# Performance work log

Hardware: AMD Instinct MI355X
Metric: run time of the kernel (lower is better)

Reference implementation:

```python
import jax, jax.numpy as jnp
import numpy as np

EPS = 1e-5

def _bn(x, g, b):
    # BatchNorm3d in training mode over (batch, spatial) dims; x: [B, C, N]
    mean = jnp.mean(x, axis=(0, 2), keepdims=True)
    var = jnp.var(x, axis=(0, 2), keepdims=True)
    return g[None, :, None] * (x - mean) * jax.lax.rsqrt(var + EPS) + b[None, :, None]


def setup_inputs() -> dict:
    key = jax.random.key(0)
    ks = jax.random.split(key, 6)
    B, C, N, K, H = 2, 128, 32768, 9, 512
    x = jax.random.normal(ks[0], (B, C, N, 1), dtype=jnp.float32)
    edge_index = jax.random.randint(ks[1], (2, B, N, K), 0, N, dtype=jnp.int32)
    s = 0.05
    return {
        "x": x,
        "edge_index": edge_index,
        "w_mr": jax.random.normal(ks[2], (C, 2 * C), dtype=jnp.float32) * s,
        "b_mr": jnp.zeros((C,), jnp.float32),
        "g_mr": jnp.ones((C,), jnp.float32),
        "be_mr": jnp.zeros((C,), jnp.float32),
        "w1": jax.random.normal(ks[3], (H, C), dtype=jnp.float32) * s,
        "b1": jnp.zeros((H,), jnp.float32),
        "g1": jnp.ones((H,), jnp.float32),
        "be1": jnp.zeros((H,), jnp.float32),
        "w2": jax.random.normal(ks[4], (C, H), dtype=jnp.float32) * s,
        "b2": jnp.zeros((C,), jnp.float32),
        "g2": jnp.ones((C,), jnp.float32),
        "be2": jnp.zeros((C,), jnp.float32),
    }


def reference(x, edge_index, w_mr, b_mr, g_mr, be_mr, w1, b1, g1, be1, w2, b2, g2, be2):
    # x: [B, C, N, 1], edge_index: [2, B, N, K]
    B, C, N, _ = x.shape
    x2 = x[..., 0]  # [B, C, N]

    # batched_index_select: gather node features along N for each (B, N, K) index
    gather = jax.vmap(lambda xb, ib: xb[:, ib])  # ([C,N],[N,K]) -> [C,N,K]
    x_i = gather(x2, edge_index[1])  # [B, C, N, K] center features
    x_j = gather(x2, edge_index[0])  # [B, C, N, K] neighbor features
    rel = jnp.max(x_j - x_i, axis=-1)  # max-relative reduction -> [B, C, N]

    # torch.cat([x.unsqueeze(2), rel.unsqueeze(2)], 2).reshape(B, 2C, N): interleaved channels
    feat = jnp.stack([x2, rel], axis=2).reshape(B, 2 * C, N)

    # BasicConv([2C, C]): Conv3d 1x1 -> BN -> ReLU
    y = jnp.einsum('oc,bcn->bon', w_mr, feat) + b_mr[None, :, None]
    y = jax.nn.relu(_bn(y, g_mr, be_mr))

    # FFN: conv1x1 C->H, BN, ReLU, conv1x1 H->C, BN, residual
    h = jnp.einsum('hc,bcn->bhn', w1, y) + b1[None, :, None]
    h = jax.nn.relu(_bn(h, g1, be1))
    out = jnp.einsum('ch,bhn->bcn', w2, h) + b2[None, :, None]
    out = _bn(out, g2, be2) + y
    return out  # [B, C, N]
```

## Files before the change

kernel.cpp:

```cpp
#include <hip/hip_runtime.h>
#include <hip/hip_bf16.h>
#include <cstddef>
#include <cstdint>

#define BB 2
#define CC 128
#define NN 32768
#define KNBR 9
#define HH 512
#define PP (BB * NN)
#define TWO_C 256
#define EPSBN 1e-5f

typedef __attribute__((ext_vector_type(4))) float f32x4;
typedef __attribute__((ext_vector_type(8))) short s16x8;

__device__ __forceinline__ float bf2f(unsigned int u) {
    return __uint_as_float(u << 16);
}
__device__ __forceinline__ unsigned short f2bf(float f) {
    unsigned int u = __float_as_uint(f);
    u += 0x7fffu + ((u >> 16) & 1u);
    return (unsigned short)(u >> 16);
}


__global__ __launch_bounds__(256) void transpose_kernel(
    const float* __restrict__ x, unsigned short* __restrict__ xT) {
    __shared__ float t[32][129];
    const int b = blockIdx.y;
    const int n0 = blockIdx.x * 32;
    const int tid = threadIdx.x;
    {
        const int tn = tid % 32;
        const int cq = tid / 32;
        for (int c = cq; c < CC; c += 8)
            t[tn][c] = x[((size_t)b * CC + c) * NN + n0 + tn];
    }
    __syncthreads();
    {
        const int ct = tid % 128;
        const int nq = tid / 128;
        for (int nl = nq; nl < 32; nl += 2)
            xT[((size_t)b * NN + n0 + nl) * CC + ct] = f2bf(t[nl][ct]);
    }
}

__global__ __launch_bounds__(256) void gather_kernel(
    const unsigned short* __restrict__ xT, const int* __restrict__ ei,
    unsigned short* __restrict__ feat) {
    __shared__ unsigned short lds[16 * 264];
    const int p0 = blockIdx.x * 16;
    const int b = p0 >> 15;
    const int n0 = p0 & (NN - 1);
    const int tid = threadIdx.x;
    const int wv = tid >> 6, lane = tid & 63;
    const unsigned short* xb = xT + (size_t)b * NN * CC;

#pragma unroll
    for (int q = 0; q < 4; q++) {
        const int pl = wv * 4 + q;
        const int n = n0 + pl;
        const int* e0 = ei + ((size_t)b * NN + n) * KNBR;
        const int* e1 = ei + ((size_t)(BB + b) * NN + n) * KNBR;
        const unsigned int xv = *(const unsigned int*)(xb + (size_t)n * CC + lane * 2);
        float m0 = -INFINITY, m1 = -INFINITY;
#pragma unroll
        for (int k = 0; k < KNBR; k++) {
            const int j0 = e0[k], j1 = e1[k];
            const unsigned int va = *(const unsigned int*)(xb + (size_t)j0 * CC + lane * 2);
            const unsigned int vb = *(const unsigned int*)(xb + (size_t)j1 * CC + lane * 2);
            m0 = fmaxf(m0, bf2f(va & 0xffffu) - bf2f(vb & 0xffffu));
            m1 = fmaxf(m1, bf2f(va >> 16) - bf2f(vb >> 16));
        }
        ushort4 o;
        o.x = (unsigned short)(xv & 0xffffu);
        o.y = f2bf(m0);
        o.z = (unsigned short)(xv >> 16);
        o.w = f2bf(m1);
        *(ushort4*)(lds + pl * 264 + lane * 4) = o;
    }
    __syncthreads();
#pragma unroll
    for (int pass = 0; pass < 2; pass++) {
        const int s = pass * 256 + tid;
        const int kt = s >> 6, ln = s & 63;
        const int pl = ln & 15, kq = ln >> 4;
        const s16x8 v = *(const s16x8*)(lds + pl * 264 + kt * 32 + kq * 8);
        *(s16x8*)(feat + ((size_t)((p0 >> 4) * 8 + kt) * 64 + ln) * 8) = v;
    }
}

__global__ __launch_bounds__(256) void wconv_kernel(
    const float* __restrict__ w_mr, const float* __restrict__ w1,
    const float* __restrict__ w2, unsigned short* __restrict__ o_mr,
    unsigned short* __restrict__ o1, unsigned short* __restrict__ o2) {
    const int t = blockIdx.x * 256 + threadIdx.x;
    const float* src; unsigned short* dst; int K; int slot;
    if (t < 8192) { src = w1; dst = o1; K = 128; slot = t; }
    else if (t < 16384) { src = w2; dst = o2; K = 512; slot = t - 8192; }
    else if (t < 20480) { src = w_mr; dst = o_mr; K = 256; slot = t - 16384; }
    else return;
    const int lane = slot & 63;
    const int kt = (slot >> 6) % (K / 32);
    const int ot = (slot >> 6) / (K / 32);
    const int oc = ot * 16 + (lane & 15);
    const int k0 = kt * 32 + (lane >> 4) * 8;
    s16x8 v;
#pragma unroll
    for (int j = 0; j < 8; j++) v[j] = (short)f2bf(src[(size_t)oc * K + k0 + j]);
    *(s16x8*)(dst + (size_t)slot * 8) = v;
}

template <int KTOT, int OC, bool ACT>
__global__ __launch_bounds__(256) void fgemm_kernel(
    const unsigned short* __restrict__ A,
    const unsigned short* __restrict__ W,
    const float* __restrict__ bias,
    const float* __restrict__ act,
    unsigned short* __restrict__ Cout,
    float* __restrict__ stats) {
    constexpr int KT = KTOT / 32;
    constexpr int OCT = OC / 32;
    __shared__ unsigned short ctile[4][2][64][8];
    __shared__ float bsA[256], bsB[256];

    const int tid = threadIdx.x;
    const int pb = blockIdx.x * 128;
    const int ob = blockIdx.y * 128;
    const int w = tid >> 6, wr = w >> 1, wc = w & 1;
    const int lane = tid & 63;
    const int lm = lane & 15, lg = lane >> 4;

    const unsigned short* Abase =
        A + ((size_t)((pb >> 4) + wr * 4) * KT * 64 + lane) * 8;
    const unsigned short* Wbase =
        W + ((size_t)((ob >> 4) + wc * 4) * KT * 64 + lane) * 8;

    f32x4 acc[4][4] = {};

    for (int kt = 0; kt < KT; kt++) {
        s16x8 aF[4], bF[4];
#pragma unroll
        for (int n = 0; n < 4; n++)
            bF[n] = *(const s16x8*)(Wbase + ((size_t)n * KT + kt) * 512);
        f32x4 sa0, sa1, sb0, sb1;
        if (ACT) {
            const int ke = kt * 32 + lg * 8;
            sa0 = *(const f32x4*)(act + ke);
            sa1 = *(const f32x4*)(act + ke + 4);
            sb0 = *(const f32x4*)(act + KTOT + ke);
            sb1 = *(const f32x4*)(act + KTOT + ke + 4);
        }
#pragma unroll
        for (int m = 0; m < 4; m++) {
            s16x8 v = *(const s16x8*)(Abase + ((size_t)m * KT + kt) * 512);
            if (ACT) {
                union { s16x8 s; __hip_bfloat162 h[4]; } u;
                u.s = v;
#pragma unroll
                for (int q = 0; q < 4; q++) {
                    const float2 f = __bfloat1622float2(u.h[q]);
                    const float slo = (q < 2) ? sa0[2 * q] : sa1[2 * q - 4];
                    const float shi = (q < 2) ? sa0[2 * q + 1] : sa1[2 * q - 3];
                    const float tlo = (q < 2) ? sb0[2 * q] : sb1[2 * q - 4];
                    const float thi = (q < 2) ? sb0[2 * q + 1] : sb1[2 * q - 3];
                    const float rlo = fmaxf(fmaf(slo, f.x, tlo), 0.f);
                    const float rhi = fmaxf(fmaf(shi, f.y, thi), 0.f);
                    u.h[q] = __float22bfloat162_rn(make_float2(rlo, rhi));
                }
                v = u.s;
            }
            aF[m] = v;
        }
#pragma unroll
        for (int m = 0; m < 4; m++)
#pragma unroll
            for (int n = 0; n < 4; n++)
                acc[m][n] = __builtin_amdgcn_mfma_f32_16x16x32_bf16(
                    aF[m], bF[n], acc[m][n], 0, 0, 0);
    }

    float sA[4] = {0.f, 0.f, 0.f, 0.f};
    float sB[4] = {0.f, 0.f, 0.f, 0.f};
    float bo[4];
#pragma unroll
    for (int n = 0; n < 4; n++) bo[n] = bias[ob + wc * 64 + n * 16 + lm];
    const int octile0 = (ob >> 5) + wc * 2;
    const int elem = lm & 7;
#pragma unroll
    for (int m = 0; m < 4; m++) {
#pragma unroll
        for (int n = 0; n < 4; n++) {
            const int tile = n >> 1;
            const int lbase = ((n & 1) * 2 + (lm >> 3)) * 16 + lg * 4;
#pragma unroll
            for (int j = 0; j < 4; j++) {
                const float h = acc[m][n][j] + bo[n];
                sA[n] += h;
                sB[n] = fmaf(h, h, sB[n]);
                ctile[w][tile][lbase + j][elem] = f2bf(h);
            }
        }
        const int ptile = (pb >> 4) + wr * 4 + m;
#pragma unroll
        for (int tile = 0; tile < 2; tile++) {
            const s16x8 v = *(const s16x8*)&ctile[w][tile][lane][0];
            *(s16x8*)(Cout + ((size_t)(ptile * OCT + octile0 + tile) * 64 + lane) * 8) = v;
        }
    }
#pragma unroll
    for (int n = 0; n < 4; n++) {
        float a = sA[n], q = sB[n];
        a += __shfl_xor(a, 16); a += __shfl_xor(a, 32);
        q += __shfl_xor(q, 16); q += __shfl_xor(q, 32);
        if (lg == 0) {
            bsA[wr * 128 + wc * 64 + n * 16 + lm] = a;
            bsB[wr * 128 + wc * 64 + n * 16 + lm] = q;
        }
    }
    __syncthreads();
    if (tid < 128) {
        atomicAdd(&stats[ob + tid], bsA[tid] + bsA[128 + tid]);
        atomicAdd(&stats[OC + ob + tid], bsB[tid] + bsB[128 + tid]);
    }
}

__global__ void finalize_kernel(const float* __restrict__ stats,
                                const float* __restrict__ g,
                                const float* __restrict__ be,
                                float* __restrict__ act, int CH, float invP) {
    const int c = blockIdx.x * blockDim.x + threadIdx.x;
    if (c < CH) {
        const float mean = stats[c] * invP;
        const float var = stats[CH + c] * invP - mean * mean;
        const float a = g[c] * rsqrtf(var + EPSBN);
        act[c] = a;
        act[CH + c] = be[c] - mean * a;
    }
}

__global__ __launch_bounds__(256) void final_kernel(
    const unsigned short* __restrict__ yF, const unsigned short* __restrict__ oF,
    const float* __restrict__ act1, const float* __restrict__ act3,
    float* __restrict__ out) {
    __shared__ float t[32][132];
    const int p0 = blockIdx.x * 32;
    const int b = p0 >> 15;
    const int n0 = p0 & (NN - 1);
    const int tid = threadIdx.x;
#pragma unroll
    for (int s = tid; s < 512; s += 256) {
        const int pt = s >> 8;
        const int kt = (s >> 6) & 3;
        const int lane = s & 63;
        const int nl = pt * 16 + (lane & 15);
        const int c0 = kt * 32 + (lane >> 4) * 8;
        const size_t off = ((size_t)(((p0 >> 4) + pt) * 4 + kt) * 64 + lane) * 8;
        const s16x8 yv = *(const s16x8*)(yF + off);
        const s16x8 ov = *(const s16x8*)(oF + off);
        const f32x4 a1lo = *(const f32x4*)(act1 + c0);
        const f32x4 a1hi = *(const f32x4*)(act1 + c0 + 4);
        const f32x4 b1lo = *(const f32x4*)(act1 + CC + c0);
        const f32x4 b1hi = *(const f32x4*)(act1 + CC + c0 + 4);
        const f32x4 a3lo = *(const f32x4*)(act3 + c0);
        const f32x4 a3hi = *(const f32x4*)(act3 + c0 + 4);
        const f32x4 b3lo = *(const f32x4*)(act3 + CC + c0);
        const f32x4 b3hi = *(const f32x4*)(act3 + CC + c0 + 4);
#pragma unroll
        for (int j = 0; j < 8; j++) {
            const float yf = bf2f((unsigned short)yv[j]);
            const float of = bf2f((unsigned short)ov[j]);
            const float a1 = (j < 4) ? a1lo[j] : a1hi[j - 4];
            const float b1 = (j < 4) ? b1lo[j] : b1hi[j - 4];
            const float a3 = (j < 4) ? a3lo[j] : a3hi[j - 4];
            const float b3 = (j < 4) ? b3lo[j] : b3hi[j - 4];
            t[nl][c0 + j] = fmaf(a3, of, b3) + fmaxf(fmaf(a1, yf, b1), 0.f);
        }
    }
    __syncthreads();
    const int tn = tid & 31;
    const int cq = tid >> 5;
    for (int c = cq; c < CC; c += 8)
        out[((size_t)b * CC + c) * NN + n0 + tn] = t[tn][c];
}

extern "C" void kernel_launch(void* const* d_in, const int* in_sizes, int n_in,
                              void* d_out, int out_size, void* d_ws, size_t ws_size,
                              hipStream_t stream) {
    const float* x     = (const float*)d_in[0];
    const int*   ei    = (const int*)d_in[1];
    const float* w_mr  = (const float*)d_in[2];
    const float* b_mr  = (const float*)d_in[3];
    const float* g_mr  = (const float*)d_in[4];
    const float* be_mr = (const float*)d_in[5];
    const float* w1    = (const float*)d_in[6];
    const float* b1    = (const float*)d_in[7];
    const float* g1    = (const float*)d_in[8];
    const float* be1   = (const float*)d_in[9];
    const float* w2    = (const float*)d_in[10];
    const float* b2    = (const float*)d_in[11];
    const float* g2    = (const float*)d_in[12];
    const float* be2   = (const float*)d_in[13];
    float* out = (float*)d_out;

    char* ws = (char*)d_ws;
    unsigned short* xT    = (unsigned short*)(ws + 0);
    unsigned short* featF = (unsigned short*)(ws + 16777216);
    unsigned short* yF    = (unsigned short*)(ws + 50331648);
    unsigned short* hF    = (unsigned short*)(ws + 67108864);
    unsigned short* oF    = (unsigned short*)(ws + 134217728);
    unsigned short* wmrF  = (unsigned short*)(ws + 150994944);
    unsigned short* w1F   = (unsigned short*)(ws + 151060480);
    unsigned short* w2F   = (unsigned short*)(ws + 151191552);
    float* stats1 = (float*)(ws + 151322624);
    float* stats2 = (float*)(ws + 151323648);
    float* stats3 = (float*)(ws + 151327744);
    float* act1   = (float*)(ws + 151328768);
    float* act2   = (float*)(ws + 151329792);
    float* act3   = (float*)(ws + 151333888);

    const float invP = 1.0f / (float)PP;

    hipMemsetAsync(stats1, 0, 6144, stream);

    transpose_kernel<<<dim3(NN / 32, BB), 256, 0, stream>>>(x, xT);
    gather_kernel<<<PP / 16, 256, 0, stream>>>(xT, ei, featF);
    wconv_kernel<<<80, 256, 0, stream>>>(w_mr, w1, w2, wmrF, w1F, w2F);

    fgemm_kernel<TWO_C, CC, false><<<dim3(PP / 128, 1), 256, 0, stream>>>(
        featF, wmrF, b_mr, act1, yF, stats1);
    finalize_kernel<<<1, CC, 0, stream>>>(stats1, g_mr, be_mr, act1, CC, invP);

    fgemm_kernel<CC, HH, true><<<dim3(PP / 128, HH / 128), 256, 0, stream>>>(
        yF, w1F, b1, act1, hF, stats2);
    finalize_kernel<<<1, HH, 0, stream>>>(stats2, g1, be1, act2, HH, invP);

    fgemm_kernel<HH, CC, true><<<dim3(PP / 128, 1), 256, 0, stream>>>(
        hF, w2F, b2, act2, oF, stats3);
    finalize_kernel<<<1, CC, 0, stream>>>(stats3, g2, be2, act3, CC, invP);

    final_kernel<<<PP / 32, 256, 0, stream>>>(yF, oF, act1, act3, out);
}
```

Measured before the change: 176.7 us.

## Stage weights in LDS, retile GEMM warps, replace atomic BN stats with partial sums

Rewrites the fused GEMM so that each block stages its weight slice in shared memory and each wave owns two 16-row point tiles across the full output-channel block, with multiple M iterations per block. It also replaces the global atomicAdd BN statistics and memset with per-block partial sums reduced by a separate reduce kernel. The third GEMM restages weights per K-quarter with extra barriers. The aim is to cut redundant global weight loads and atomic contention, at the cost of more LDS usage, more synchronisation, and extra partial-sum memory traffic.

Result: slower. 256.4 us (+45.1%).

```diff
diff --git a/kernel.cpp b/kernel.cpp
--- a/kernel.cpp
+++ b/kernel.cpp
@@ -22,6 +22,23 @@
     unsigned int u = __float_as_uint(f);
     u += 0x7fffu + ((u >> 16) & 1u);
     return (unsigned short)(u >> 16);
+}
+
+__device__ __forceinline__ s16x8 bnrelu(s16x8 v, f32x4 sa0, f32x4 sa1,
+                                        f32x4 sb0, f32x4 sb1) {
+    union { s16x8 s; __hip_bfloat162 h[4]; } u;
+    u.s = v;
+#pragma unroll
+    for (int q = 0; q < 4; q++) {
+        const float2 f = __bfloat1622float2(u.h[q]);
+        const float slo = (q < 2) ? sa0[2 * q] : sa1[2 * q - 4];
+        const float shi = (q < 2) ? sa0[2 * q + 1] : sa1[2 * q - 3];
+        const float tlo = (q < 2) ? sb0[2 * q] : sb1[2 * q - 4];
+        const float thi = (q < 2) ? sb0[2 * q + 1] : sb1[2 * q - 3];
+        u.h[q] = __float22bfloat162_rn(make_float2(
+            fmaxf(fmaf(slo, f.x, tlo), 0.f), fmaxf(fmaf(shi, f.y, thi), 0.f)));
+    }
+    return u.s;
 }
 
 
@@ -112,131 +129,160 @@
     *(s16x8*)(dst + (size_t)slot * 8) = v;
 }
 
-template <int KTOT, int OC, bool ACT>
-__global__ __launch_bounds__(256) void fgemm_kernel(
+template <int KTOT, int OCB, int OC, bool ACT, bool RESTAGE, int MITERS>
+__global__ __launch_bounds__(256, 2) void wgemm_kernel(
     const unsigned short* __restrict__ A,
     const unsigned short* __restrict__ W,
     const float* __restrict__ bias,
     const float* __restrict__ act,
     unsigned short* __restrict__ Cout,
-    float* __restrict__ stats) {
+    float* __restrict__ part) {
     constexpr int KT = KTOT / 32;
-    constexpr int OCT = OC / 32;
-    __shared__ unsigned short ctile[4][2][64][8];
-    __shared__ float bsA[256], bsB[256];
+    constexpr int KQ = KT / 4;
+    constexpr int NT = OCB / 16;
+    constexpr int NT2 = NT / 2;
+    constexpr int WTILES = RESTAGE ? NT * 4 : NT * KT;
+    constexpr int OCT32 = OC / 32;
+    __shared__ __align__(16) unsigned short WL[WTILES * 512];
+    __shared__ __align__(16) unsigned short ctile[4][NT2][64][8];
+    __shared__ float bs[4][2][OCB];
 
     const int tid = threadIdx.x;
-    const int pb = blockIdx.x * 128;
-    const int ob = blockIdx.y * 128;
-    const int w = tid >> 6, wr = w >> 1, wc = w & 1;
+    const int w = tid >> 6;
     const int lane = tid & 63;
     const int lm = lane & 15, lg = lane >> 4;
-
-    const unsigned short* Abase =
-        A + ((size_t)((pb >> 4) + wr * 4) * KT * 64 + lane) * 8;
-    const unsigned short* Wbase =
-        W + ((size_t)((ob >> 4) + wc * 4) * KT * 64 + lane) * 8;
-
-    f32x4 acc[4][4] = {};
-
-    for (int kt = 0; kt < KT; kt++) {
-        s16x8 aF[4], bF[4];
-#pragma unroll
-        for (int n = 0; n < 4; n++)
-            bF[n] = *(const s16x8*)(Wbase + ((size_t)n * KT + kt) * 512);
-        f32x4 sa0, sa1, sb0, sb1;
-        if (ACT) {
-            const int ke = kt * 32 + lg * 8;
-            sa0 = *(const f32x4*)(act + ke);
-            sa1 = *(const f32x4*)(act + ke + 4);
-            sb0 = *(const f32x4*)(act + KTOT + ke);
-            sb1 = *(const f32x4*)(act + KTOT + ke + 4);
-        }
-#pragma unroll
-        for (int m = 0; m < 4; m++) {
-            s16x8 v = *(const s16x8*)(Abase + ((size_t)m * KT + kt) * 512);
-            if (ACT) {
-                union { s16x8 s; __hip_bfloat162 h[4]; } u;
-                u.s = v;
-#pragma unroll
-                for (int q = 0; q < 4; q++) {
-                    const float2 f = __bfloat1622float2(u.h[q]);
-                    const float slo = (q < 2) ? sa0[2 * q] : sa1[2 * q - 4];
-                    const float shi = (q < 2) ? sa0[2 * q + 1] : sa1[2 * q - 3];
-                    const float tlo = (q < 2) ? sb0[2 * q] : sb1[2 * q - 4];
-                    const float thi = (q < 2) ? sb0[2 * q + 1] : sb1[2 * q - 3];
-                    const float rlo = fmaxf(fmaf(slo, f.x, tlo), 0.f);
-                    const float rhi = fmaxf(fmaf(shi, f.y, thi), 0.f);
-                    u.h[q] = __float22bfloat162_rn(make_float2(rlo, rhi));
+    const int pb = blockIdx.x * (MITERS * 128);
+    const int ob = blockIdx.y * OCB;
+
+    if (!RESTAGE) {
+        for (int s = tid; s < WTILES * 64; s += 256) {
+            const int t = s >> 6, ln = s & 63;
+            const int n = t / KT, ktg = t % KT;
+            *(s16x8*)(WL + t * 512 + ln * 8) =
+                *(const s16x8*)(W + ((size_t)(((ob >> 4) + n) * KT + ktg) * 64 + ln) * 8);
+        }
+        __syncthreads();
+    }
+
+    float sA[NT], sB[NT];
+#pragma unroll
+    for (int n = 0; n < NT; n++) { sA[n] = 0.f; sB[n] = 0.f; }
+
+    for (int iter = 0; iter < MITERS; iter++) {
+        const int ptile0 = (pb >> 4) + (iter * 4 + w) * 2;
+        f32x4 acc[2][NT] = {};
+
+        for (int kq = 0; kq < KQ; kq++) {
+            s16x8 a0[4], a1[4];
+#pragma unroll
+            for (int kt = 0; kt < 4; kt++) {
+                const int ktg = kq * 4 + kt;
+                a0[kt] = *(const s16x8*)(A + ((size_t)(ptile0 * KT + ktg) * 64 + lane) * 8);
+                a1[kt] = *(const s16x8*)(A + ((size_t)((ptile0 + 1) * KT + ktg) * 64 + lane) * 8);
+            }
+            if (RESTAGE) {
+                __syncthreads();
+                for (int s = tid; s < NT * 4 * 64; s += 256) {
+                    const int t = s >> 6, ln = s & 63;
+                    const int n = t >> 2, ktl = t & 3;
+                    *(s16x8*)(WL + t * 512 + ln * 8) =
+                        *(const s16x8*)(W + ((size_t)(((ob >> 4) + n) * KT + kq * 4 + ktl) * 64 + ln) * 8);
                 }
-                v = u.s;
-            }
-            aF[m] = v;
-        }
-#pragma unroll
-        for (int m = 0; m < 4; m++)
-#pragma unroll
-            for (int n = 0; n < 4; n++)
-                acc[m][n] = __builtin_amdgcn_mfma_f32_16x16x32_bf16(
-                    aF[m], bF[n], acc[m][n], 0, 0, 0);
-    }
-
-    float sA[4] = {0.f, 0.f, 0.f, 0.f};
-    float sB[4] = {0.f, 0.f, 0.f, 0.f};
-    float bo[4];
-#pragma unroll
-    for (int n = 0; n < 4; n++) bo[n] = bias[ob + wc * 64 + n * 16 + lm];
-    const int octile0 = (ob >> 5) + wc * 2;
-    const int elem = lm & 7;
-#pragma unroll
-    for (int m = 0; m < 4; m++) {
-#pragma unroll
-        for (int n = 0; n < 4; n++) {
-            const int tile = n >> 1;
-            const int lbase = ((n & 1) * 2 + (lm >> 3)) * 16 + lg * 4;
-#pragma unroll
-            for (int j = 0; j < 4; j++) {
-                const float h = acc[m][n][j] + bo[n];
-                sA[n] += h;
-                sB[n] = fmaf(h, h, sB[n]);
-                ctile[w][tile][lbase + j][elem] = f2bf(h);
-            }
-        }
-        const int ptile = (pb >> 4) + wr * 4 + m;
-#pragma unroll
-        for (int tile = 0; tile < 2; tile++) {
-            const s16x8 v = *(const s16x8*)&ctile[w][tile][lane][0];
-            *(s16x8*)(Cout + ((size_t)(ptile * OCT + octile0 + tile) * 64 + lane) * 8) = v;
-        }
-    }
-#pragma unroll
-    for (int n = 0; n < 4; n++) {
+                __syncthreads();
+            }
+#pragma unroll
+            for (int kt = 0; kt < 4; kt++) {
+                s16x8 t0 = a0[kt], t1 = a1[kt];
+                if (ACT) {
+                    const int ke = kq * 128 + kt * 32 + lg * 8;
+                    const f32x4 xa0 = *(const f32x4*)(act + ke);
+                    const f32x4 xa1 = *(const f32x4*)(act + ke + 4);
+                    const f32x4 xb0 = *(const f32x4*)(act + KTOT + ke);
+                    const f32x4 xb1 = *(const f32x4*)(act + KTOT + ke + 4);
+                    t0 = bnrelu(t0, xa0, xa1, xb0, xb1);
+                    t1 = bnrelu(t1, xa0, xa1, xb0, xb1);
+                }
+#pragma unroll
+                for (int n = 0; n < NT; n++) {
+                    const int t = RESTAGE ? (n * 4 + kt) : (n * KT + kq * 4 + kt);
+                    const s16x8 bF = *(const s16x8*)(WL + t * 512 + lane * 8);
+                    acc[0][n] = __builtin_amdgcn_mfma_f32_16x16x32_bf16(
+                        t0, bF, acc[0][n], 0, 0, 0);
+                    acc[1][n] = __builtin_amdgcn_mfma_f32_16x16x32_bf16(
+                        t1, bF, acc[1][n], 0, 0, 0);
+                }
+            }
+        }
+
+        float bo[NT];
+#pragma unroll
+        for (int n = 0; n < NT; n++) bo[n] = bias[ob + n * 16 + lm];
+#pragma unroll
+        for (int m = 0; m < 2; m++) {
+            const int ptile = ptile0 + m;
+#pragma unroll
+            for (int n = 0; n < NT; n++) {
+                const int og = n >> 1;
+                const int lbase = ((n & 1) * 2 + (lm >> 3)) * 16 + lg * 4;
+                const int elem = lm & 7;
+#pragma unroll
+                for (int j = 0; j < 4; j++) {
+                    const float h = acc[m][n][j] + bo[n];
+                    sA[n] += h;
+                    sB[n] = fmaf(h, h, sB[n]);
+                    ctile[w][og][lbase + j][elem] = f2bf(h);
+                }
+            }
+#pragma unroll
+            for (int og = 0; og < NT2; og++) {
+                const s16x8 v = *(const s16x8*)&ctile[w][og][lane][0];
+                *(s16x8*)(Cout +
+                          ((size_t)(ptile * OCT32 + (ob >> 5) + og) * 64 + lane) * 8) = v;
+            }
+        }
+    }
+
+#pragma unroll
+    for (int n = 0; n < NT; n++) {
         float a = sA[n], q = sB[n];
         a += __shfl_xor(a, 16); a += __shfl_xor(a, 32);
         q += __shfl_xor(q, 16); q += __shfl_xor(q, 32);
-        if (lg == 0) {
-            bsA[wr * 128 + wc * 64 + n * 16 + lm] = a;
-            bsB[wr * 128 + wc * 64 + n * 16 + lm] = q;
-        }
-    }
-    __syncthreads();
-    if (tid < 128) {
-        atomicAdd(&stats[ob + tid], bsA[tid] + bsA[128 + tid]);
-        atomicAdd(&stats[OC + ob + tid], bsB[tid] + bsB[128 + tid]);
-    }
-}
-
-__global__ void finalize_kernel(const float* __restrict__ stats,
-                                const float* __restrict__ g,
-                                const float* __restrict__ be,
-                                float* __restrict__ act, int CH, float invP) {
-    const int c = blockIdx.x * blockDim.x + threadIdx.x;
-    if (c < CH) {
-        const float mean = stats[c] * invP;
-        const float var = stats[CH + c] * invP - mean * mean;
+        if (lg == 0) { bs[w][0][n * 16 + lm] = a; bs[w][1][n * 16 + lm] = q; }
+    }
+    __syncthreads();
+    if (tid < OCB) {
+        const float s = bs[0][0][tid] + bs[1][0][tid] + bs[2][0][tid] + bs[3][0][tid];
+        const float q = bs[0][1][tid] + bs[1][1][tid] + bs[2][1][tid] + bs[3][1][tid];
+        const size_t o = (size_t)(blockIdx.y * gridDim.x + blockIdx.x) * 2 * OCB;
+        part[o + tid] = s;
+        part[o + OCB + tid] = q;
+    }
+}
+
+template <int OCB, int GX>
+__global__ __launch_bounds__(256) void reduce_kernel(
+    const float* __restrict__ part, const float* __restrict__ g,
+    const float* __restrict__ be, float* __restrict__ act, int OC, float invP) {
+    __shared__ float ls[4][64], lq[4][64];
+    const int cl = threadIdx.x & 63, rl = threadIdx.x >> 6;
+    const int c = blockIdx.x * 64 + cl;
+    const int by = c / OCB, co = c % OCB;
+    float s = 0.f, q = 0.f;
+    for (int bx = rl; bx < GX; bx += 4) {
+        const size_t o = (size_t)(by * GX + bx) * 2 * OCB;
+        s += part[o + co];
+        q += part[o + OCB + co];
+    }
+    ls[rl][cl] = s; lq[rl][cl] = q;
+    __syncthreads();
+    if (rl == 0) {
+        s = ls[0][cl] + ls[1][cl] + ls[2][cl] + ls[3][cl];
+        q = lq[0][cl] + lq[1][cl] + lq[2][cl] + lq[3][cl];
+        const float mean = s * invP;
+        const float var = q * invP - mean * mean;
         const float a = g[c] * rsqrtf(var + EPSBN);
         act[c] = a;
-        act[CH + c] = be[c] - mean * a;
+        act[OC + c] = be[c] - mean * a;
     }
 }
 
@@ -313,32 +359,33 @@
     unsigned short* wmrF  = (unsigned short*)(ws + 150994944);
     unsigned short* w1F   = (unsigned short*)(ws + 151060480);
     unsigned short* w2F   = (unsigned short*)(ws + 151191552);
-    float* stats1 = (float*)(ws + 151322624);
-    float* stats2 = (float*)(ws + 151323648);
-    float* stats3 = (float*)(ws + 151327744);
-    float* act1   = (float*)(ws + 151328768);
-    float* act2   = (float*)(ws + 151329792);
-    float* act3   = (float*)(ws + 151333888);
+    float* act1  = (float*)(ws + 151322624);
+    float* act2  = (float*)(ws + 151323648);
+    float* act3  = (float*)(ws + 151327744);
+    float* part1 = (float*)(ws + 151328768);
+    float* part2 = (float*)(ws + 151590912);
+    float* part3 = (float*)(ws + 152639488);
 
     const float invP = 1.0f / (float)PP;
-
-    hipMemsetAsync(stats1, 0, 6144, stream);
 
     transpose_kernel<<<dim3(NN / 32, BB), 256, 0, stream>>>(x, xT);
     gather_kernel<<<PP / 16, 256, 0, stream>>>(xT, ei, featF);
     wconv_kernel<<<80, 256, 0, stream>>>(w_mr, w1, w2, wmrF, w1F, w2F);
 
-    fgemm_kernel<TWO_C, CC, false><<<dim3(PP / 128, 1), 256, 0, stream>>>(
-        featF, wmrF, b_mr, act1, yF, stats1);
-    finalize_kernel<<<1, CC, 0, stream>>>(stats1, g_mr, be_mr, act1, CC, invP);
-
-    fgemm_kernel<CC, HH, true><<<dim3(PP / 128, HH / 128), 256, 0, stream>>>(
-        yF, w1F, b1, act1, hF, stats2);
-    finalize_kernel<<<1, HH, 0, stream>>>(stats2, g1, be1, act2, HH, invP);
-
-    fgemm_kernel<HH, CC, true><<<dim3(PP / 128, 1), 256, 0, stream>>>(
-        hF, w2F, b2, act2, oF, stats3);
-    finalize_kernel<<<1, CC, 0, stream>>>(stats3, g2, be2, act3, CC, invP);
+    wgemm_kernel<TWO_C, 64, CC, false, false, 2>
+        <<<dim3(PP / 256, 2), 256, 0, stream>>>(featF, wmrF, b_mr, act1, yF, part1);
+    reduce_kernel<64, PP / 256><<<CC / 64, 256, 0, stream>>>(
+        part1, g_mr, be_mr, act1, CC, invP);
+
+    wgemm_kernel<CC, 128, HH, true, false, 2>
+        <<<dim3(PP / 256, 4), 256, 0, stream>>>(yF, w1F, b1, act1, hF, part2);
+    reduce_kernel<128, PP / 256><<<HH / 64, 256, 0, stream>>>(
+        part2, g1, be1, act2, HH, invP);
+
+    wgemm_kernel<HH, 128, CC, true, true, 1>
+        <<<dim3(PP / 128, 1), 256, 0, stream>>>(hF, w2F, b2, act2, oF, part3);
+    reduce_kernel<128, PP / 128><<<CC / 64, 256, 0, stream>>>(
+        part3, g2, be2, act3, CC, invP);
 
     final_kernel<<<PP / 32, 256, 0, stream>>>(yF, oF, act1, act3, out);
 }
```
